# Kernel optimization log

Hardware: AMD Instinct MI355X
Metric: run time of the kernel (lower is better)

The kernel has to match this reference:

```python
import jax, jax.numpy as jnp
import numpy as np

N, E, K, IN, OUT = 20000, 320000, 5, 256, 128
NAN_FRAC = 0.3


def setup_inputs() -> dict:
    key = jax.random.key(0)
    ks = jax.random.split(key, 8)
    x = jax.random.normal(ks[0], (N, IN), dtype=jnp.float32)
    nan_mask = jax.random.uniform(ks[1], (N, IN)) < NAN_FRAC
    x = jnp.where(nan_mask, jnp.nan, x)  # missing features as NaN
    edge_index = jax.random.randint(ks[2], (2, E), 0, N, dtype=jnp.int64)
    logp = jax.nn.log_softmax(jax.random.normal(ks[3], (K,), dtype=jnp.float32))
    means = jax.random.normal(ks[4], (K, IN), dtype=jnp.float32)
    logvars = jax.random.normal(ks[5], (K, IN), dtype=jnp.float32) * 0.1
    xav = 1.414 * np.sqrt(6.0 / (IN + OUT))
    weight = jax.random.uniform(ks[6], (IN, OUT), dtype=jnp.float32, minval=-xav, maxval=xav)
    bias = jnp.zeros((OUT,), dtype=jnp.float32)
    return {"x": x, "edge_index": edge_index, "logp": logp, "means": means,
            "logvars": logvars, "weight": weight, "bias": bias}


def _ex_relu(mu, sigma):
    # E[relu(X)] for X ~ N(mu, sigma); sigma is the variance
    sigma_s = jnp.where(sigma == 0, 1e-10, sigma)
    ss = jnp.sqrt(sigma_s)
    w = mu / ss
    nr = ss * (jnp.exp(-0.5 * w * w) / np.sqrt(2 * np.pi)
               + 0.5 * w * (1.0 + jax.lax.erf(w / np.sqrt(2))))
    return jnp.where(sigma == 0, jnp.maximum(mu, 0.0), nr)


def _gcn_norm(edge_index, num_nodes):
    # add self-loops, symmetric D^-1/2 A D^-1/2 normalization
    row = jnp.concatenate([edge_index[0], jnp.arange(num_nodes, dtype=edge_index.dtype)])
    col = jnp.concatenate([edge_index[1], jnp.arange(num_nodes, dtype=edge_index.dtype)])
    ones = jnp.ones(row.shape[0], dtype=jnp.float32)
    deg = jax.ops.segment_sum(ones, row, num_segments=num_nodes)
    dinv = jnp.where(deg > 0, jax.lax.rsqrt(deg), 0.0)
    wn = dinv[row] * dinv[col]
    return row, col, wn


def reference(x, edge_index, logp, means, logvars, weight, bias):
    n = x.shape[0]
    dim = x.shape[1]
    row, col, wn = _gcn_norm(edge_index, n)
    wn2 = wn * wn  # adj2 = adj * adj (elementwise on sparse values)

    isnan = jnp.isnan(x)                                       # [N, IN]
    variances = jnp.exp(logvars)                               # [K, IN]
    mean_mat = jnp.where(isnan[None], means[:, None, :], x[None])      # [K, N, IN]
    var_mat = jnp.where(isnan[None], variances[:, None, :], 0.0)       # [K, N, IN]

    transform_x = jnp.einsum('kni,io->kno', mean_mat, weight) + bias   # [K, N, OUT]
    transform_covs = jnp.einsum('kni,io->kno', var_mat, weight * weight)

    def spmm(vals, X):  # segment-sum SpMM: out[r] += vals_e * X[c]
        return jax.ops.segment_sum(X[col] * vals[:, None], row, num_segments=n)

    conv_x = jax.vmap(lambda X: spmm(wn, X))(transform_x)      # [K, N, OUT]
    conv_covs = jax.vmap(lambda X: spmm(wn2, X))(transform_covs)

    expected_x = _ex_relu(conv_x, conv_covs)                   # [K, N, OUT]

    # GMM responsibilities per node
    log_n = (-0.5 * jnp.sum((mean_mat - means[:, None, :]) ** 2 / variances[:, None, :], axis=2)
             - 0.5 * dim * np.log(2 * np.pi) - 0.5 * jnp.sum(logvars))  # [K, N]
    gamma = jax.nn.softmax(logp[:, None] + log_n, axis=0)      # [K, N]

    return jnp.sum(expected_x * gamma[:, :, None], axis=0)     # [N, OUT]
```

## Files before the change

### kernel.cpp

```cpp
#include <hip/hip_runtime.h>
#include <stdint.h>

#define N_NODES 20000
#define N_EDGES 320000
#define K_MIX 5
#define IN_F 256
#define OUT_F 128
#define NT 11
#define TC (NT * OUT_F)

typedef __attribute__((ext_vector_type(8))) short short8;
typedef __attribute__((ext_vector_type(4))) float floatx4;

__device__ __forceinline__ float bf2f(unsigned int u) {
  union { unsigned int i; float f; } v;
  v.i = (u & 0xffffu) << 16;
  return v.f;
}
__device__ __forceinline__ unsigned short f2bf(float f) {
  union { float f; unsigned int i; } v;
  v.f = f;
  unsigned int x = v.i;
  unsigned int r = (x + 0x7fffu + ((x >> 16) & 1u)) >> 16;
  return (unsigned short)r;
}

__device__ __forceinline__ float exrelu(float mu, float sig) {
  if (sig < 1e-30f) return fmaxf(mu, 0.f);
  float ss = sqrtf(sig);
  float w = mu / ss;
  float e = __expf(-0.5f * w * w);
  float axv = fabsf(w) * 0.70710678118654752f;
  float t = 1.f / (1.f + 0.3275911f * axv);
  float poly = t * (0.254829592f +
              t * (-0.284496736f +
              t * (1.421413741f +
              t * (-1.453152027f + t * 1.061405429f))));
  float erfv = 1.f - poly * e;
  erfv = copysignf(erfv, w);
  return ss * (e * 0.3989422804014327f + 0.5f * w * (1.f + erfv));
}

__device__ __forceinline__ void gll16(const void* g, void* l) {
  __builtin_amdgcn_global_load_lds(
      (const __attribute__((address_space(1))) void*)g,
      (__attribute__((address_space(3))) void*)l, 16, 0, 0);
}

__global__ void k_deg(const int* __restrict__ row, int* __restrict__ deg) {
  int t = blockIdx.x * 256 + threadIdx.x;
  if (t < N_EDGES) atomicAdd(&deg[row[t]], 1);
}

__global__ void k_scan1(const int* __restrict__ deg, int* __restrict__ startofs,
                        int* __restrict__ bsums, float* __restrict__ dinv) {
  __shared__ int sd[256];
  int t = threadIdx.x;
  int i = blockIdx.x * 256 + t;
  int v = (i < N_NODES) ? deg[i] : 0;
  if (i < N_NODES) dinv[i] = rsqrtf((float)(v + 1));
  sd[t] = v;
  __syncthreads();
  for (int off = 1; off < 256; off <<= 1) {
    int u = (t >= off) ? sd[t - off] : 0;
    __syncthreads();
    sd[t] += u;
    __syncthreads();
  }
  if (i < N_NODES) startofs[i] = sd[t] - v;
  if (t == 255) bsums[blockIdx.x] = sd[255];
}

__global__ void k_scan2(int* __restrict__ bsums, int nb) {
  __shared__ int sd[128];
  int t = threadIdx.x;
  int v = (t < nb) ? bsums[t] : 0;
  sd[t] = v;
  __syncthreads();
  for (int off = 1; off < 128; off <<= 1) {
    int u = (t >= off) ? sd[t - off] : 0;
    __syncthreads();
    sd[t] += u;
    __syncthreads();
  }
  if (t < nb) bsums[t] = sd[t] - v;
}

__global__ void k_scan3(int* __restrict__ startofs, int* __restrict__ cursor,
                        const int* __restrict__ bsums) {
  int i = blockIdx.x * 256 + threadIdx.x;
  if (i < N_NODES) {
    int s0 = startofs[i] + bsums[blockIdx.x];
    startofs[i] = s0;
    cursor[i] = s0;
  }
}

__global__ void k_scatter(const int* __restrict__ row, const int* __restrict__ col,
                          const float* __restrict__ dinv, int* __restrict__ cursor,
                          int* __restrict__ csr_col, float* __restrict__ csr_w) {
  int t = blockIdx.x * 256 + threadIdx.x;
  if (t < N_EDGES) {
    int r = row[t], c = col[t];
    int p = atomicAdd(&cursor[r], 1);
    csr_col[p] = c;
    csr_w[p] = dinv[r] * dinv[c];
  }
}

__global__ void k_buildB(const float* __restrict__ W, const float* __restrict__ means,
                         const float* __restrict__ logvars, unsigned short* __restrict__ Bt) {
  int idx = blockIdx.x * 256 + threadIdx.x;
  int j = idx >> 15;
  int rem = idx & 32767;
  int n = rem >> 8;
  int kk = rem & 255;
  float wv = W[kk * OUT_F + n];
  float val;
  if (j == 0) val = wv;
  else if (j <= 5) val = means[(j - 1) * IN_F + kk] * wv;
  else val = expf(logvars[(j - 6) * IN_F + kk]) * wv * wv;
  Bt[idx] = f2bf(val);
}

__global__ void k_prepx(const float* __restrict__ x, const float* __restrict__ logp,
                        const float* __restrict__ means, const float* __restrict__ logvars,
                        unsigned short* __restrict__ X0, float* __restrict__ gamma) {
  __shared__ float s_mean[K_MIX * IN_F];
  __shared__ float s_rv[K_MIX * IN_F];
  int t = threadIdx.x;
  for (int j = t; j < K_MIX * IN_F; j += 256) {
    s_mean[j] = means[j];
    s_rv[j] = expf(-logvars[j]);
  }
  __syncthreads();
  int node = blockIdx.x * 4 + (t >> 6);
  if (node >= N_NODES) return;
  int lane = t & 63;
  float4 xv = *(const float4*)(x + (size_t)node * IN_F + 4 * lane);
  float xf[4] = {xv.x, xv.y, xv.z, xv.w};
  float gsum[K_MIX] = {0, 0, 0, 0, 0};
  ushort4 o;
  unsigned short* op = (unsigned short*)&o;
#pragma unroll
  for (int j = 0; j < 4; j++) {
    bool nn = (xf[j] != xf[j]);
    op[j] = nn ? (unsigned short)0x7FC0 : f2bf(xf[j]);
    if (!nn) {
      int fi = 4 * lane + j;
#pragma unroll
      for (int k = 0; k < K_MIX; k++) {
        float d = xf[j] - s_mean[k * IN_F + fi];
        gsum[k] += d * d * s_rv[k * IN_F + fi];
      }
    }
  }
  *(ushort4*)(X0 + node * IN_F + 4 * lane) = o;
#pragma unroll
  for (int k = 0; k < K_MIX; k++)
    for (int off = 32; off; off >>= 1) gsum[k] += __shfl_xor(gsum[k], off, 64);
  if (lane == 0) {
    float lg[K_MIX], mx = -1e30f;
#pragma unroll
    for (int k = 0; k < K_MIX; k++) {
      lg[k] = logp[k] - 0.5f * gsum[k];
      mx = fmaxf(mx, lg[k]);
    }
    float se = 0.f;
#pragma unroll
    for (int k = 0; k < K_MIX; k++) { lg[k] = expf(lg[k] - mx); se += lg[k]; }
    float inv = 1.f / se;
#pragma unroll
    for (int k = 0; k < K_MIX; k++) gamma[node * K_MIX + k] = lg[k] * inv;
  }
}

__global__ __launch_bounds__(64) void k_spmm(const unsigned short* __restrict__ X0,
                       const int* __restrict__ startofs, const int* __restrict__ deg,
                       const float* __restrict__ dinv, const int* __restrict__ csr_col,
                       const float* __restrict__ csr_w, unsigned short* __restrict__ G,
                       float* __restrict__ sArr) {
  int node = blockIdx.x;
  int lane = threadIdx.x;
  int fo = 4 * lane;
  float ax[4] = {0, 0, 0, 0}, am[4] = {0, 0, 0, 0}, am2[4] = {0, 0, 0, 0};
  float ssum = 0.f;
  float ws = dinv[node];
  ws = ws * ws;
  int st = startofs[node];
  int total = deg[node] + 1;
  ushort4 zero4 = {0, 0, 0, 0};
  ushort4 B0 = zero4, B1 = zero4, B2 = zero4, B3 = zero4,
          B4 = zero4, B5 = zero4, B6 = zero4, B7 = zero4;
  float W0 = 0.f, W1 = 0.f, W2 = 0.f, W3 = 0.f,
        W4 = 0.f, W5 = 0.f, W6 = 0.f, W7 = 0.f;
  B0 = *(const ushort4*)(X0 + node * IN_F + fo); W0 = ws;
#define PFILL(S)                                                      \
  if (S < total) {                                                    \
    int c = csr_col[st + (S - 1)];                                    \
    W##S = csr_w[st + (S - 1)];                                       \
    B##S = *(const ushort4*)(X0 + c * IN_F + fo);                     \
  }
  PFILL(1) PFILL(2) PFILL(3) PFILL(4) PFILL(5) PFILL(6) PFILL(7)
#undef PFILL

#define STEP(S)                                                       \
  if (W##S != 0.f) {                                                  \
    float wv = W##S, wv2 = wv * wv;                                   \
    ssum += wv;                                                       \
    const unsigned short* xp = (const unsigned short*)&B##S;          \
    _Pragma("unroll")                                                 \
    for (int j = 0; j < 4; j++) {                                     \
      float xf = bf2f(xp[j]);                                         \
      bool nn = (xf != xf);                                           \
      ax[j] = fmaf(wv, nn ? 0.f : xf, ax[j]);                         \
      am[j] += nn ? wv : 0.f;                                         \
      am2[j] += nn ? wv2 : 0.f;                                       \
    }                                                                 \
  }                                                                   \
  if (base + 8 + S < total) {                                         \
    int c = csr_col[st + base + 7 + S];                               \
    W##S = csr_w[st + base + 7 + S];                                  \
    B##S = *(const ushort4*)(X0 + c * IN_F + fo);                     \
  } else {                                                            \
    W##S = 0.f;                                                       \
  }

  for (int base = 0; base < total; base += 8) {
    STEP(0) STEP(1) STEP(2) STEP(3) STEP(4) STEP(5) STEP(6) STEP(7)
  }
#undef STEP

  ushort4 o;
  o.x = f2bf(ax[0]); o.y = f2bf(ax[1]); o.z = f2bf(ax[2]); o.w = f2bf(ax[3]);
  *(ushort4*)(G + node * 768 + fo) = o;
  o.x = f2bf(am[0]); o.y = f2bf(am[1]); o.z = f2bf(am[2]); o.w = f2bf(am[3]);
  *(ushort4*)(G + node * 768 + 256 + fo) = o;
  o.x = f2bf(am2[0]); o.y = f2bf(am2[1]); o.z = f2bf(am2[2]); o.w = f2bf(am2[3]);
  *(ushort4*)(G + node * 768 + 512 + fo) = o;
  if (lane == 0) sArr[node] = ssum;
}

__global__ __launch_bounds__(256) void k_gemm(const unsigned short* __restrict__ G,
                                              const unsigned short* __restrict__ Bt,
                                              unsigned short* __restrict__ T) {
  __shared__ __align__(16) char Als[128 * 64 * 2];
  __shared__ __align__(16) char Bls[128 * 64 * 2];
  int mt = blockIdx.x, jt = blockIdx.y;
  int aoff = (jt == 0) ? 0 : (jt <= 5 ? 256 : 512);
  int t = threadIdx.x, w = t >> 6, lane = t & 63;
  int wr = w >> 1, wc = w & 1;
  int quad = lane >> 4, l16 = lane & 15;
  const unsigned short* Bp = Bt + (size_t)jt * 32768;

  floatx4 acc[4][4];
  floatx4 z = {0.f, 0.f, 0.f, 0.f};
#pragma unroll
  for (int mi = 0; mi < 4; mi++)
#pragma unroll
    for (int ni = 0; ni < 4; ni++) acc[mi][ni] = z;

  for (int k0 = 0; k0 < 256; k0 += 64) {
    __syncthreads();
#pragma unroll
    for (int i = 0; i < 4; i++) {
      int r = i * 32 + w * 8 + (lane >> 3);
      int c = (lane & 7) ^ (r & 7);
      int gr = mt * 128 + r;
      if (gr >= N_NODES) gr = N_NODES - 1;
      gll16(G + (size_t)gr * 768 + aoff + k0 + c * 8, Als + i * 4096 + w * 1024);
      gll16(Bp + (size_t)r * 256 + k0 + c * 8, Bls + i * 4096 + w * 1024);
    }
    __syncthreads();
#pragma unroll
    for (int ks = 0; ks < 2; ks++) {
      int cc = ks * 4 + quad;
      short8 a[4], b[4];
#pragma unroll
      for (int mi = 0; mi < 4; mi++) {
        int r = wr * 64 + mi * 16 + l16;
        a[mi] = *(const short8*)(Als + r * 128 + (cc ^ (r & 7)) * 16);
      }
#pragma unroll
      for (int ni = 0; ni < 4; ni++) {
        int r = wc * 64 + ni * 16 + l16;
        b[ni] = *(const short8*)(Bls + r * 128 + (cc ^ (r & 7)) * 16);
      }
#pragma unroll
      for (int mi = 0; mi < 4; mi++)
#pragma unroll
        for (int ni = 0; ni < 4; ni++)
          acc[mi][ni] = __builtin_amdgcn_mfma_f32_16x16x32_bf16(a[mi], b[ni], acc[mi][ni], 0, 0, 0);
    }
  }
#pragma unroll
  for (int mi = 0; mi < 4; mi++)
#pragma unroll
    for (int ni = 0; ni < 4; ni++) {
      int gc = jt * 128 + wc * 64 + ni * 16 + l16;
#pragma unroll
      for (int reg = 0; reg < 4; reg++) {
        int gr = mt * 128 + wr * 64 + mi * 16 + quad * 4 + reg;
        if (gr < N_NODES) T[(size_t)gr * TC + gc] = f2bf(acc[mi][ni][reg]);
      }
    }
}

__global__ void k_final(const unsigned short* __restrict__ T, const float* __restrict__ gamma,
                        const float* __restrict__ sArr, const float* __restrict__ bias,
                        float* __restrict__ out) {
  int t = threadIdx.x;
  int node = blockIdx.x * 4 + (t >> 6);
  if (node >= N_NODES) return;
  int lane = t & 63;
  int o0 = 2 * lane;
  float g[K_MIX];
#pragma unroll
  for (int k = 0; k < K_MIX; k++) g[k] = gamma[node * K_MIX + k];
  float sv = sArr[node];
  float b0 = bias[o0], b1 = bias[o0 + 1];
  const unsigned short* Tr = T + (size_t)node * TC;
  unsigned int c0u = *(const unsigned int*)(Tr + o0);
  float cx0 = bf2f(c0u), cx1 = bf2f(c0u >> 16);
  float a0 = 0.f, a1 = 0.f;
#pragma unroll
  for (int k = 0; k < K_MIX; k++) {
    unsigned int tm = *(const unsigned int*)(Tr + 128 * (1 + k) + o0);
    unsigned int tv = *(const unsigned int*)(Tr + 128 * (6 + k) + o0);
    float mu0 = cx0 + bf2f(tm) + b0 * sv;
    float mu1 = cx1 + bf2f(tm >> 16) + b1 * sv;
    a0 += g[k] * exrelu(mu0, bf2f(tv));
    a1 += g[k] * exrelu(mu1, bf2f(tv >> 16));
  }
  float2 ov = {a0, a1};
  *(float2*)(out + (size_t)node * OUT_F + o0) = ov;
}

extern "C" void kernel_launch(void* const* d_in, const int* in_sizes, int n_in,
                              void* d_out, int out_size, void* d_ws, size_t ws_size,
                              hipStream_t stream) {
  const float* x = (const float*)d_in[0];
  const int* ei = (const int*)d_in[1];
  const float* logp = (const float*)d_in[2];
  const float* means = (const float*)d_in[3];
  const float* lvar = (const float*)d_in[4];
  const float* W = (const float*)d_in[5];
  const float* bias = (const float*)d_in[6];
  float* out = (float*)d_out;
  const int* row = ei;
  const int* col = ei + N_EDGES;

  char* p = (char*)d_ws;
  auto alloc = [&](size_t bytes) -> char* {
    char* q = p;
    p += (bytes + 255) & ~((size_t)255);
    return q;
  };
  int* deg = (int*)alloc(N_NODES * 4);
  float* dinv = (float*)alloc(N_NODES * 4);
  int* startofs = (int*)alloc(N_NODES * 4);
  int* cursor = (int*)alloc(N_NODES * 4);
  int* bsums = (int*)alloc(128 * 4);
  int* csr_col = (int*)alloc((size_t)N_EDGES * 4);
  float* csr_w = (float*)alloc((size_t)N_EDGES * 4);
  float* gamma = (float*)alloc((size_t)N_NODES * K_MIX * 4);
  float* sArr = (float*)alloc(N_NODES * 4);
  unsigned short* Bt = (unsigned short*)alloc((size_t)NT * 128 * 256 * 2);
  unsigned short* X0 = (unsigned short*)alloc((size_t)N_NODES * IN_F * 2);
  unsigned short* G = (unsigned short*)alloc((size_t)N_NODES * 768 * 2);
  unsigned short* T = (unsigned short*)alloc((size_t)N_NODES * TC * 2);

  hipMemsetAsync(deg, 0, N_NODES * 4, stream);
  k_deg<<<(N_EDGES + 255) / 256, 256, 0, stream>>>(row, deg);
  k_scan1<<<79, 256, 0, stream>>>(deg, startofs, bsums, dinv);
  k_scan2<<<1, 128, 0, stream>>>(bsums, 79);
  k_scan3<<<79, 256, 0, stream>>>(startofs, cursor, bsums);
  k_scatter<<<(N_EDGES + 255) / 256, 256, 0, stream>>>(row, col, dinv, cursor, csr_col, csr_w);
  k_buildB<<<(NT * 128 * 256) / 256, 256, 0, stream>>>(W, means, lvar, Bt);
  k_prepx<<<N_NODES / 4, 256, 0, stream>>>(x, logp, means, lvar, X0, gamma);
  k_spmm<<<N_NODES, 64, 0, stream>>>(X0, startofs, deg, dinv, csr_col, csr_w, G, sArr);
  k_gemm<<<dim3((N_NODES + 127) / 128, NT), 256, 0, stream>>>(G, Bt, T);
  k_final<<<N_NODES / 4, 256, 0, stream>>>(T, gamma, sArr, bias, out);
}
```

Before: 227.4 us.

## Merge degree, prep and B-build into one launch; single-block degree scan

The degree atomics, the per-node feature preparation with GMM responsibilities, and the weight-matrix build are independent, so they now run as block ranges of one kernel. The three-kernel scan becomes a single 1024-thread block in which each thread scans 20 nodes serially. This cuts five launches and their serialisation gaps down to two, so the small front stages can overlap. In exchange, the blocks running the degree atomics and the B-build also reserve the prep stage's shared-memory arrays, which can lower occupancy, and the scan now runs on a single compute unit.

```diff
diff --git a/kernel.cpp b/kernel.cpp
--- a/kernel.cpp
+++ b/kernel.cpp
@@ -8,6 +8,10 @@
 #define OUT_F 128
 #define NT 11
 #define TC (NT * OUT_F)
+
+#define DEG_BLOCKS (N_EDGES / 256)
+#define PREP_BLOCKS (N_NODES / 4)
+#define BUILDB_BLOCKS ((NT * 128 * 256) / 256)
 
 typedef __attribute__((ext_vector_type(8))) short short8;
 typedef __attribute__((ext_vector_type(4))) float floatx4;
@@ -47,70 +51,71 @@
       (__attribute__((address_space(3))) void*)l, 16, 0, 0);
 }
 
-__global__ void k_deg(const int* __restrict__ row, int* __restrict__ deg) {
-  int t = blockIdx.x * 256 + threadIdx.x;
-  if (t < N_EDGES) atomicAdd(&deg[row[t]], 1);
-}
-
-__global__ void k_scan1(const int* __restrict__ deg, int* __restrict__ startofs,
-                        int* __restrict__ bsums, float* __restrict__ dinv) {
-  __shared__ int sd[256];
+__global__ __launch_bounds__(256) void k_front(
+    const int* __restrict__ row, int* __restrict__ deg,
+    const float* __restrict__ x, const float* __restrict__ logp,
+    const float* __restrict__ means, const float* __restrict__ logvars,
+    const float* __restrict__ W, unsigned short* __restrict__ X0,
+    float* __restrict__ gamma, unsigned short* __restrict__ Bt) {
+  __shared__ float s_mean[K_MIX * IN_F];
+  __shared__ float s_rv[K_MIX * IN_F];
+  int b = blockIdx.x;
   int t = threadIdx.x;
-  int i = blockIdx.x * 256 + t;
-  int v = (i < N_NODES) ? deg[i] : 0;
-  if (i < N_NODES) dinv[i] = rsqrtf((float)(v + 1));
-  sd[t] = v;
-  __syncthreads();
-  for (int off = 1; off < 256; off <<= 1) {
-    int u = (t >= off) ? sd[t - off] : 0;
-    __syncthreads();
-    sd[t] += u;
-    __syncthreads();
-  }
-  if (i < N_NODES) startofs[i] = sd[t] - v;
-  if (t == 255) bsums[blockIdx.x] = sd[255];
-}
-
-__global__ void k_scan2(int* __restrict__ bsums, int nb) {
-  __shared__ int sd[128];
-  int t = threadIdx.x;
-  int v = (t < nb) ? bsums[t] : 0;
-  sd[t] = v;
-  __syncthreads();
-  for (int off = 1; off < 128; off <<= 1) {
-    int u = (t >= off) ? sd[t - off] : 0;
-    __syncthreads();
-    sd[t] += u;
-    __syncthreads();
-  }
-  if (t < nb) bsums[t] = sd[t] - v;
-}
-
-__global__ void k_scan3(int* __restrict__ startofs, int* __restrict__ cursor,
-                        const int* __restrict__ bsums) {
-  int i = blockIdx.x * 256 + threadIdx.x;
-  if (i < N_NODES) {
-    int s0 = startofs[i] + bsums[blockIdx.x];
-    startofs[i] = s0;
-    cursor[i] = s0;
-  }
-}
-
-__global__ void k_scatter(const int* __restrict__ row, const int* __restrict__ col,
-                          const float* __restrict__ dinv, int* __restrict__ cursor,
-                          int* __restrict__ csr_col, float* __restrict__ csr_w) {
-  int t = blockIdx.x * 256 + threadIdx.x;
-  if (t < N_EDGES) {
-    int r = row[t], c = col[t];
-    int p = atomicAdd(&cursor[r], 1);
-    csr_col[p] = c;
-    csr_w[p] = dinv[r] * dinv[c];
-  }
-}
-
-__global__ void k_buildB(const float* __restrict__ W, const float* __restrict__ means,
-                         const float* __restrict__ logvars, unsigned short* __restrict__ Bt) {
-  int idx = blockIdx.x * 256 + threadIdx.x;
+
+  if (b < DEG_BLOCKS) {
+    int e = b * 256 + t;
+    atomicAdd(&deg[row[e]], 1);
+    return;
+  }
+  b -= DEG_BLOCKS;
+  if (b < PREP_BLOCKS) {
+    for (int j = t; j < K_MIX * IN_F; j += 256) {
+      s_mean[j] = means[j];
+      s_rv[j] = expf(-logvars[j]);
+    }
+    __syncthreads();
+    int node = b * 4 + (t >> 6);
+    int lane = t & 63;
+    float4 xv = *(const float4*)(x + (size_t)node * IN_F + 4 * lane);
+    float xf[4] = {xv.x, xv.y, xv.z, xv.w};
+    float gsum[K_MIX] = {0, 0, 0, 0, 0};
+    ushort4 o;
+    unsigned short* op = (unsigned short*)&o;
+#pragma unroll
+    for (int j = 0; j < 4; j++) {
+      bool nn = (xf[j] != xf[j]);
+      op[j] = nn ? (unsigned short)0x7FC0 : f2bf(xf[j]);
+      if (!nn) {
+        int fi = 4 * lane + j;
+#pragma unroll
+        for (int k = 0; k < K_MIX; k++) {
+          float d = xf[j] - s_mean[k * IN_F + fi];
+          gsum[k] += d * d * s_rv[k * IN_F + fi];
+        }
+      }
+    }
+    *(ushort4*)(X0 + node * IN_F + 4 * lane) = o;
+#pragma unroll
+    for (int k = 0; k < K_MIX; k++)
+      for (int off = 32; off; off >>= 1) gsum[k] += __shfl_xor(gsum[k], off, 64);
+    if (lane == 0) {
+      float lg[K_MIX], mx = -1e30f;
+#pragma unroll
+      for (int k = 0; k < K_MIX; k++) {
+        lg[k] = logp[k] - 0.5f * gsum[k];
+        mx = fmaxf(mx, lg[k]);
+      }
+      float se = 0.f;
+#pragma unroll
+      for (int k = 0; k < K_MIX; k++) { lg[k] = expf(lg[k] - mx); se += lg[k]; }
+      float inv = 1.f / se;
+#pragma unroll
+      for (int k = 0; k < K_MIX; k++) gamma[node * K_MIX + k] = lg[k] * inv;
+    }
+    return;
+  }
+  b -= PREP_BLOCKS;
+  int idx = b * 256 + t;
   int j = idx >> 15;
   int rem = idx & 32767;
   int n = rem >> 8;
@@ -123,55 +128,54 @@
   Bt[idx] = f2bf(val);
 }
 
-__global__ void k_prepx(const float* __restrict__ x, const float* __restrict__ logp,
-                        const float* __restrict__ means, const float* __restrict__ logvars,
-                        unsigned short* __restrict__ X0, float* __restrict__ gamma) {
-  __shared__ float s_mean[K_MIX * IN_F];
-  __shared__ float s_rv[K_MIX * IN_F];
+__global__ __launch_bounds__(1024) void k_scan(const int* __restrict__ deg,
+                                               int* __restrict__ startofs,
+                                               int* __restrict__ cursor,
+                                               float* __restrict__ dinv) {
+  __shared__ int sd[1024];
   int t = threadIdx.x;
-  for (int j = t; j < K_MIX * IN_F; j += 256) {
-    s_mean[j] = means[j];
-    s_rv[j] = expf(-logvars[j]);
-  }
+  int base = t * 20;
+  int loc[21];
+  int s = 0;
+#pragma unroll
+  for (int j = 0; j < 20; j++) {
+    int i = base + j;
+    loc[j] = s;
+    int v = (i < N_NODES) ? deg[i] : 0;
+    s += v;
+  }
+  loc[20] = s;
+  sd[t] = s;
   __syncthreads();
-  int node = blockIdx.x * 4 + (t >> 6);
-  if (node >= N_NODES) return;
-  int lane = t & 63;
-  float4 xv = *(const float4*)(x + (size_t)node * IN_F + 4 * lane);
-  float xf[4] = {xv.x, xv.y, xv.z, xv.w};
-  float gsum[K_MIX] = {0, 0, 0, 0, 0};
-  ushort4 o;
-  unsigned short* op = (unsigned short*)&o;
-#pragma unroll
-  for (int j = 0; j < 4; j++) {
-    bool nn = (xf[j] != xf[j]);
-    op[j] = nn ? (unsigned short)0x7FC0 : f2bf(xf[j]);
-    if (!nn) {
-      int fi = 4 * lane + j;
-#pragma unroll
-      for (int k = 0; k < K_MIX; k++) {
-        float d = xf[j] - s_mean[k * IN_F + fi];
-        gsum[k] += d * d * s_rv[k * IN_F + fi];
-      }
-    }
-  }
-  *(ushort4*)(X0 + node * IN_F + 4 * lane) = o;
-#pragma unroll
-  for (int k = 0; k < K_MIX; k++)
-    for (int off = 32; off; off >>= 1) gsum[k] += __shfl_xor(gsum[k], off, 64);
-  if (lane == 0) {
-    float lg[K_MIX], mx = -1e30f;
-#pragma unroll
-    for (int k = 0; k < K_MIX; k++) {
-      lg[k] = logp[k] - 0.5f * gsum[k];
-      mx = fmaxf(mx, lg[k]);
-    }
-    float se = 0.f;
-#pragma unroll
-    for (int k = 0; k < K_MIX; k++) { lg[k] = expf(lg[k] - mx); se += lg[k]; }
-    float inv = 1.f / se;
-#pragma unroll
-    for (int k = 0; k < K_MIX; k++) gamma[node * K_MIX + k] = lg[k] * inv;
+  for (int off = 1; off < 1024; off <<= 1) {
+    int u = (t >= off) ? sd[t - off] : 0;
+    __syncthreads();
+    sd[t] += u;
+    __syncthreads();
+  }
+  int tbase = sd[t] - s;
+#pragma unroll
+  for (int j = 0; j < 20; j++) {
+    int i = base + j;
+    if (i < N_NODES) {
+      int s0 = tbase + loc[j];
+      startofs[i] = s0;
+      cursor[i] = s0;
+      int v = loc[j + 1] - loc[j];
+      dinv[i] = rsqrtf((float)(v + 1));
+    }
+  }
+}
+
+__global__ void k_scatter(const int* __restrict__ row, const int* __restrict__ col,
+                          const float* __restrict__ dinv, int* __restrict__ cursor,
+                          int* __restrict__ csr_col, float* __restrict__ csr_w) {
+  int t = blockIdx.x * 256 + threadIdx.x;
+  if (t < N_EDGES) {
+    int r = row[t], c = col[t];
+    int p = atomicAdd(&cursor[r], 1);
+    csr_col[p] = c;
+    csr_w[p] = dinv[r] * dinv[c];
   }
 }
 
@@ -360,7 +364,6 @@
   float* dinv = (float*)alloc(N_NODES * 4);
   int* startofs = (int*)alloc(N_NODES * 4);
   int* cursor = (int*)alloc(N_NODES * 4);
-  int* bsums = (int*)alloc(128 * 4);
   int* csr_col = (int*)alloc((size_t)N_EDGES * 4);
   float* csr_w = (float*)alloc((size_t)N_EDGES * 4);
   float* gamma = (float*)alloc((size_t)N_NODES * K_MIX * 4);
@@ -371,13 +374,10 @@
   unsigned short* T = (unsigned short*)alloc((size_t)N_NODES * TC * 2);
 
   hipMemsetAsync(deg, 0, N_NODES * 4, stream);
-  k_deg<<<(N_EDGES + 255) / 256, 256, 0, stream>>>(row, deg);
-  k_scan1<<<79, 256, 0, stream>>>(deg, startofs, bsums, dinv);
-  k_scan2<<<1, 128, 0, stream>>>(bsums, 79);
-  k_scan3<<<79, 256, 0, stream>>>(startofs, cursor, bsums);
+  k_front<<<DEG_BLOCKS + PREP_BLOCKS + BUILDB_BLOCKS, 256, 0, stream>>>(
+      row, deg, x, logp, means, lvar, W, X0, gamma, Bt);
+  k_scan<<<1, 1024, 0, stream>>>(deg, startofs, cursor, dinv);
   k_scatter<<<(N_EDGES + 255) / 256, 256, 0, stream>>>(row, col, dinv, cursor, csr_col, csr_w);
-  k_buildB<<<(NT * 128 * 256) / 256, 256, 0, stream>>>(W, means, lvar, Bt);
-  k_prepx<<<N_NODES / 4, 256, 0, stream>>>(x, logp, means, lvar, X0, gamma);
   k_spmm<<<N_NODES, 64, 0, stream>>>(X0, startofs, deg, dinv, csr_col, csr_w, G, sArr);
   k_gemm<<<dim3((N_NODES + 127) / 128, NT), 256, 0, stream>>>(G, Bt, T);
   k_final<<<N_NODES / 4, 256, 0, stream>>>(T, gamma, sArr, bias, out);
```

New measurement: 250.2 us. 1.1x slower.
